# Optimization experiments

Measured on AMD Instinct MI355X. Metric: run time of the kernel, lower is better.

Reference implementation:

```python
import jax, jax.numpy as jnp
import numpy as np

BSZ, T, H, P, N = 2, 2048, 16, 64, 64

def setup_inputs() -> dict:
    key = jax.random.key(0)
    k1, k2, k3, k4, k5 = jax.random.split(key, 5)
    X = jax.random.normal(k1, (BSZ, T, H, P), dtype=jnp.float32)
    delta = jax.random.uniform(k2, (BSZ, T, H), dtype=jnp.float32)
    Bmat = jax.random.normal(k3, (BSZ, T, N), dtype=jnp.float32)
    Cmat = jax.random.normal(k4, (BSZ, T, N), dtype=jnp.float32)
    # module init: A_log = log(arange(1, n_heads+1))
    A_log = jnp.log(jnp.arange(1, H + 1, dtype=jnp.float32))
    return {"X": X, "delta": delta, "Bmat": Bmat, "Cmat": Cmat, "A_log": A_log}

def reference(X, delta, Bmat, Cmat, A_log):
    # X: [B,T,H,P], delta: [B,T,H], Bmat/Cmat: [B,T,N], A_log: [H]
    Bsz, Tlen, Hh, Pp = X.shape
    Nn = Bmat.shape[-1]
    dA = jnp.exp(delta * -jnp.exp(A_log))  # [B,T,H] per-step scalar decay

    def step(h, inp):
        dA_t, dt_t, X_t, B_t, C_t = inp  # [B,H], [B,H], [B,H,P], [B,N], [B,N]
        # outer-product input: delta * X outer B -> [B,H,P,N]
        dBx = (dt_t[:, :, None, None] * X_t[..., None]) * B_t[:, None, None, :]
        h = dA_t[:, :, None, None] * h + dBx
        y_t = jnp.einsum('bhpn,bn->bhp', h, C_t)
        return h, y_t

    h0 = jnp.zeros((Bsz, Hh, Pp, Nn), dtype=X.dtype)
    xs = (
        jnp.moveaxis(dA, 1, 0),    # [T,B,H]
        jnp.moveaxis(delta, 1, 0), # [T,B,H]
        jnp.moveaxis(X, 1, 0),     # [T,B,H,P]
        jnp.moveaxis(Bmat, 1, 0),  # [T,B,N]
        jnp.moveaxis(Cmat, 1, 0),  # [T,B,N]
    )
    h_last, ys = jax.lax.scan(step, h0, xs)
    y = jnp.moveaxis(ys, 0, 1)  # [B,T,H,P]
    return y, h_last
```

## Files before the change

### kernel.cpp

```cpp
#include <hip/hip_runtime.h>


constexpr int BSZ = 2, T = 2048, H = 16, P = 64, N = 64;
constexpr int L = 64, NC = T / L;
constexpr int LSB = 72;

using bf16x8 = __attribute__((ext_vector_type(8))) short;
using f32x4  = __attribute__((ext_vector_type(4))) float;

__device__ inline ushort f2bf(float f) {
    unsigned u = __float_as_uint(f);
    u += 0x7FFFu + ((u >> 16) & 1u);
    return (ushort)(u >> 16);
}
__device__ inline unsigned pack2(float a, float b) {
    return (unsigned)f2bf(a) | ((unsigned)f2bf(b) << 16);
}
__device__ inline float bf2f(ushort h) {
    return __uint_as_float(((unsigned)h) << 16);
}
__device__ inline int swz(int row, int col) {
    return row * 64 + ((((col >> 3) ^ (row & 7))) << 3) + (col & 7);
}

typedef __attribute__((address_space(3))) unsigned int       lds_u32;
typedef const __attribute__((address_space(1))) unsigned int glb_u32;
__device__ inline void dma16(const void* g, void* l) {
    __builtin_amdgcn_global_load_lds((glb_u32*)g, (lds_u32*)l, 16, 0, 0);
}
__device__ inline void dma4(const void* g, void* l) {
    __builtin_amdgcn_global_load_lds((glb_u32*)g, (lds_u32*)l, 4, 0, 0);
}

__global__ __launch_bounds__(256, 4) void ka_prep(
    const float* __restrict__ X, const float* __restrict__ delta,
    const float* __restrict__ Bm, const float* __restrict__ Cm,
    const float* __restrict__ A_log,
    ushort* __restrict__ Xtg, ushort* __restrict__ Hbuf,
    ushort* __restrict__ Bbf, ushort* __restrict__ Cbf,
    float* __restrict__ Vec, float* __restrict__ Dchunk)
{
    __shared__ __align__(16) ushort sXt[4096];
    __shared__ __align__(16) ushort sBt[64 * LSB];
    __shared__ float sWf[64];

    const int tid  = threadIdx.x, lane = tid & 63, w = tid >> 6;
    const int quad = lane >> 4,   l16  = lane & 15;
    const int blk = blockIdx.x;
    const int h   = blk & (H - 1);
    const int c   = (blk >> 4) & (NC - 1);
    const int b   = blk >> 9;
    const int t0  = c * L;
    const int chunkid = (b * H + h) * NC + c;
    const int bcid    = b * NC + c;

    {
        const float* gB = Bm + ((size_t)b * T + t0) * N;
        #pragma unroll
        for (int i = 0; i < 8; ++i) {
            int tau = (w * 8 + i) * 2;
            *(unsigned*)&sBt[lane * LSB + tau] =
                pack2(gB[(size_t)tau * N + lane], gB[(size_t)(tau + 1) * N + lane]);
        }
    }
    {
        const float* gX = X + (((size_t)b * T + t0) * H + h) * P;
        #pragma unroll
        for (int i = 0; i < 8; ++i) {
            int tau = w * 16 + 2 * i;
            *(unsigned*)&sXt[swz(lane, tau)] =
                pack2(gX[(size_t)tau * (H * P) + lane],
                      gX[(size_t)(tau + 1) * (H * P) + lane]);
        }
    }
    if (h == 0) {
        const float4* gB4 = (const float4*)(Bm + ((size_t)b * T + t0) * N);
        const float4* gC4 = (const float4*)(Cm + ((size_t)b * T + t0) * N);
        ushort* Bt = Bbf + (size_t)bcid * 4096;
        ushort* Ct = Cbf + (size_t)bcid * 4096;
        #pragma unroll
        for (int r = 0; r < 4; ++r) {
            int idx = r * 256 + tid, t = idx >> 4, n4 = idx & 15;
            int g = n4 >> 1, half = n4 & 1;
            int off = t * 64 + (((g ^ (t & 7))) << 3) + half * 4;
            float4 vb = gB4[idx], vc = gC4[idx];
            *(uint2*)&Bt[off] = make_uint2(pack2(vb.x, vb.y), pack2(vb.z, vb.w));
            *(uint2*)&Ct[off] = make_uint2(pack2(vc.x, vc.y), pack2(vc.z, vc.w));
        }
    }
    if (w == 0) {
        float dl = delta[((size_t)b * T + t0 + lane) * H + h];
        float s = -__expf(A_log[h]) * dl;
        #pragma unroll
        for (int off = 1; off < 64; off <<= 1) {
            float u = __shfl_up(s, off, 64);
            if (lane >= off) s += u;
        }
        float sL  = __shfl(s, 63, 64);
        float lnd = __logf(dl);
        sWf[lane] = __expf(sL + lnd - s);
        float* vp = Vec + (size_t)chunkid * 192;
        vp[lane]       = s;
        vp[64 + lane]  = lnd - s;
        vp[128 + lane] = __expf(s);
        if (lane == 63) Dchunk[chunkid] = __expf(sL);
    }
    __syncthreads();

    f32x4 ha[4];
    #pragma unroll
    for (int j = 0; j < 4; ++j) ha[j] = (f32x4){0.f, 0.f, 0.f, 0.f};
    #pragma unroll
    for (int ks = 0; ks < 2; ++ks) {
        const int ko = ks * 32 + quad * 8;
        const int sg = (ko >> 3) ^ (l16 & 7);
        bf16x8 xa = *(const bf16x8*)&sXt[(w * 16 + l16) * 64 + sg * 8];
        union { bf16x8 v; unsigned u[4]; } xw;
        #pragma unroll
        for (int j2 = 0; j2 < 4; ++j2)
            xw.u[j2] = pack2(bf2f((ushort)xa[2*j2])   * sWf[ko + 2*j2],
                             bf2f((ushort)xa[2*j2+1]) * sWf[ko + 2*j2+1]);
        #pragma unroll
        for (int jn = 0; jn < 4; ++jn) {
            bf16x8 bb = *(const bf16x8*)&sBt[(jn * 16 + l16) * LSB + ko];
            ha[jn] = __builtin_amdgcn_mfma_f32_16x16x32_bf16(xw.v, bb, ha[jn], 0, 0, 0);
        }
    }

    {
        ushort* Xtt = Xtg + (size_t)chunkid * 4096;
        #pragma unroll
        for (int i = 0; i < 2; ++i) {
            int j = i * 256 + tid;
            ((uint4*)Xtt)[j] = ((const uint4*)sXt)[j];
        }
    }
    __syncthreads();
    {
        ushort* hst = sBt;
        #pragma unroll
        for (int jn = 0; jn < 4; ++jn)
            #pragma unroll
            for (int r = 0; r < 4; ++r)
                hst[swz(w * 16 + quad * 4 + r, jn * 16 + l16)] = f2bf(ha[jn][r]);
    }
    __syncthreads();
    {
        ushort* Ht = Hbuf + (size_t)chunkid * 4096;
        #pragma unroll
        for (int i = 0; i < 2; ++i) {
            int j = i * 256 + tid;
            ((uint4*)Ht)[j] = ((const uint4*)sBt)[j];
        }
    }
}

__global__ __launch_bounds__(256, 4) void k2_scan(
    const float* __restrict__ Dchunk, ushort* __restrict__ Hbuf,
    float* __restrict__ Hlast)
{
    const unsigned gid = blockIdx.x * 256u + threadIdx.x;
    const int bh  = gid >> 11;
    const int rem = gid & 2047;
    unsigned* Hb = (unsigned*)Hbuf;
    unsigned v[NC];
    #pragma unroll
    for (int cc = 0; cc < NC; ++cc)
        v[cc] = Hb[(size_t)(bh * NC + cc) * 2048 + rem];
    float hx = 0.f, hy = 0.f;
    #pragma unroll
    for (int cc = 0; cc < NC; ++cc) {
        const float lo = bf2f((ushort)(v[cc] & 0xffffu));
        const float hi = bf2f((ushort)(v[cc] >> 16));
        v[cc] = pack2(hx, hy);
        const float D = Dchunk[bh * NC + cc];
        hx = D * hx + lo;
        hy = D * hy + hi;
    }
    #pragma unroll
    for (int cc = 0; cc < NC; ++cc)
        Hb[(size_t)(bh * NC + cc) * 2048 + rem] = v[cc];
    const int p   = rem >> 5, w32 = rem & 31;
    const int g   = (w32 >> 2) ^ (p & 7);
    const int n0  = (g << 3) + ((w32 & 3) << 1);
    *(float2*)&Hlast[(size_t)bh * 4096 + p * 64 + n0] = make_float2(hx, hy);
}

__global__ __launch_bounds__(256, 4) void k3_y(
    const ushort* __restrict__ Xtg, const ushort* __restrict__ Bbf,
    const ushort* __restrict__ Cbf, const float* __restrict__ Vec,
    const ushort* __restrict__ Hbuf, float* __restrict__ Y)
{
    __shared__ __align__(16) ushort sC [4096];
    __shared__ __align__(16) ushort sB [4096];
    __shared__ __align__(16) ushort sXt[4096];
    __shared__ __align__(16) ushort sH [4096];
    __shared__ float sVec[192];

    const int tid  = threadIdx.x, lane = tid & 63, w = tid >> 6;
    const int quad = lane >> 4,   l16  = lane & 15;
    const int blk = blockIdx.x;
    const int h   = blk & (H - 1);
    const int c   = (blk >> 4) & (NC - 1);
    const int b   = blk >> 9;
    const int t0  = c * L;
    const int chunkid = (b * H + h) * NC + c;
    const int bcid    = b * NC + c;

    {
        const ushort* gsrc;
        ushort* ldst;
        if      (w == 0) { gsrc = Cbf + (size_t)bcid * 4096;    ldst = sC;  }
        else if (w == 1) { gsrc = Bbf + (size_t)bcid * 4096;    ldst = sB;  }
        else if (w == 2) { gsrc = Xtg + (size_t)chunkid * 4096; ldst = sXt; }
        else             { gsrc = Hbuf + (size_t)chunkid * 4096; ldst = sH; }
        const char* g = (const char*)gsrc + lane * 16;
        #pragma unroll
        for (int i = 0; i < 8; ++i)
            dma16(g + i * 1024, (char*)ldst + i * 1024);
        if (w == 0) {
            const float* vp = Vec + (size_t)chunkid * 192;
            dma4(vp + lane,       sVec);
            dma4(vp + 64 + lane,  sVec + 64);
            dma4(vp + 128 + lane, sVec + 128);
        }
    }
    __syncthreads();

    f32x4 g4[4];
    #pragma unroll
    for (int j = 0; j < 4; ++j) g4[j] = (f32x4){0.f, 0.f, 0.f, 0.f};
    #pragma unroll
    for (int ks = 0; ks < 2; ++ks) {
        const int ko = ks * 32 + quad * 8;
        const int sg = (ko >> 3) ^ (l16 & 7);
        bf16x8 af = *(const bf16x8*)&sC[(w * 16 + l16) * 64 + sg * 8];
        #pragma unroll
        for (int jt = 0; jt < 4; ++jt) {
            bf16x8 bfr = *(const bf16x8*)&sB[(jt * 16 + l16) * 64 + sg * 8];
            g4[jt] = __builtin_amdgcn_mfma_f32_16x16x32_bf16(af, bfr, g4[jt], 0, 0, 0);
        }
    }
    __syncthreads();

    #pragma unroll
    for (int jt = 0; jt < 4; ++jt) {
        const int tau = jt * 16 + l16;
        const float sbv = sVec[64 + tau];
        #pragma unroll
        for (int r = 0; r < 4; ++r) {
            const int t = w * 16 + quad * 4 + r;
            float arg = (tau <= t) ? (sVec[t] + sbv) : -80.0f;
            sB[swz(t, tau)] = f2bf(__expf(arg) * g4[jt][r]);
        }
    }
    __syncthreads();

    f32x4 ya[4], acc[4];
    #pragma unroll
    for (int j = 0; j < 4; ++j) {
        ya[j]  = (f32x4){0.f, 0.f, 0.f, 0.f};
        acc[j] = (f32x4){0.f, 0.f, 0.f, 0.f};
    }
    #pragma unroll
    for (int ks = 0; ks < 2; ++ks) {
        const int ko = ks * 32 + quad * 8;
        const int sg = (ko >> 3) ^ (l16 & 7);
        bf16x8 sa = *(const bf16x8*)&sB[(w * 16 + l16) * 64 + sg * 8];
        bf16x8 ca = *(const bf16x8*)&sC[(w * 16 + l16) * 64 + sg * 8];
        #pragma unroll
        for (int jp = 0; jp < 4; ++jp) {
            bf16x8 xb = *(const bf16x8*)&sXt[(jp * 16 + l16) * 64 + sg * 8];
            bf16x8 hb = *(const bf16x8*)&sH [(jp * 16 + l16) * 64 + sg * 8];
            ya[jp]  = __builtin_amdgcn_mfma_f32_16x16x32_bf16(sa, xb, ya[jp], 0, 0, 0);
            acc[jp] = __builtin_amdgcn_mfma_f32_16x16x32_bf16(ca, hb, acc[jp], 0, 0, 0);
        }
    }

    float* Yg = Y + (((size_t)b * T + t0) * H + h) * P;
    #pragma unroll
    for (int jp = 0; jp < 4; ++jp)
        #pragma unroll
        for (int r = 0; r < 4; ++r) {
            const int t = w * 16 + quad * 4 + r;
            Yg[(size_t)t * (H * P) + jp * 16 + l16] =
                ya[jp][r] + sVec[128 + t] * acc[jp][r];
        }
}

extern "C" void kernel_launch(void* const* d_in, const int* in_sizes, int n_in,
                              void* d_out, int out_size, void* d_ws, size_t ws_size,
                              hipStream_t stream) {
    const float* X     = (const float*)d_in[0];
    const float* delta = (const float*)d_in[1];
    const float* Bm    = (const float*)d_in[2];
    const float* Cm    = (const float*)d_in[3];
    const float* A_log = (const float*)d_in[4];

    float* Y     = (float*)d_out;
    float* Hlast = (float*)d_out + (size_t)BSZ * T * H * P;

    char* ws = (char*)d_ws;
    ushort* Hbuf = (ushort*)(ws);
    ushort* Xtg  = (ushort*)(ws + (8u << 20));
    ushort* Bbf  = (ushort*)(ws + (16u << 20));
    ushort* Cbf  = (ushort*)(ws + (16u << 20) + (512u << 10));
    float*  Vec  = (float*)(ws + (17u << 20));
    float*  Dchunk = (float*)(ws + (18u << 20));

    const int nblk = BSZ * NC * H;
    ka_prep<<<nblk, 256, 0, stream>>>(X, delta, Bm, Cm, A_log,
                                      Xtg, Hbuf, Bbf, Cbf, Vec, Dchunk);
    k2_scan<<<256, 256, 0, stream>>>(Dchunk, Hbuf, Hlast);
    k3_y<<<nblk, 256, 0, stream>>>(Xtg, Bbf, Cbf, Vec, Hbuf, Y);
}
```

Measured before the change: 95.55 us.

## Fold inter-chunk state scan into the output kernel, removing separate scan launch

The separate chunk-state scan kernel is removed. Each output block now recomputes its own incoming state by accumulating the decayed per-chunk states of all earlier chunks directly from the workspace. The last chunk also produces the final hidden state. This saves a kernel launch and the global read-modify-write of the state buffer, but adds redundant work that grows with chunk index (quadratic in the number of chunks), which creates load imbalance across blocks.

```diff
diff --git a/kernel.cpp b/kernel.cpp
--- a/kernel.cpp
+++ b/kernel.cpp
@@ -137,59 +137,25 @@
     }
     __syncthreads();
     {
-        ushort* hst = sBt;
         #pragma unroll
         for (int jn = 0; jn < 4; ++jn)
             #pragma unroll
             for (int r = 0; r < 4; ++r)
-                hst[swz(w * 16 + quad * 4 + r, jn * 16 + l16)] = f2bf(ha[jn][r]);
+                sBt[swz(w * 16 + quad * 4 + r, jn * 16 + l16)] = f2bf(ha[jn][r]);
     }
     __syncthreads();
     {
         ushort* Ht = Hbuf + (size_t)chunkid * 4096;
-        #pragma unroll
-        for (int i = 0; i < 2; ++i) {
-            int j = i * 256 + tid;
-            ((uint4*)Ht)[j] = ((const uint4*)sBt)[j];
-        }
-    }
-}
-
-__global__ __launch_bounds__(256, 4) void k2_scan(
-    const float* __restrict__ Dchunk, ushort* __restrict__ Hbuf,
-    float* __restrict__ Hlast)
-{
-    const unsigned gid = blockIdx.x * 256u + threadIdx.x;
-    const int bh  = gid >> 11;
-    const int rem = gid & 2047;
-    unsigned* Hb = (unsigned*)Hbuf;
-    unsigned v[NC];
-    #pragma unroll
-    for (int cc = 0; cc < NC; ++cc)
-        v[cc] = Hb[(size_t)(bh * NC + cc) * 2048 + rem];
-    float hx = 0.f, hy = 0.f;
-    #pragma unroll
-    for (int cc = 0; cc < NC; ++cc) {
-        const float lo = bf2f((ushort)(v[cc] & 0xffffu));
-        const float hi = bf2f((ushort)(v[cc] >> 16));
-        v[cc] = pack2(hx, hy);
-        const float D = Dchunk[bh * NC + cc];
-        hx = D * hx + lo;
-        hy = D * hy + hi;
-    }
-    #pragma unroll
-    for (int cc = 0; cc < NC; ++cc)
-        Hb[(size_t)(bh * NC + cc) * 2048 + rem] = v[cc];
-    const int p   = rem >> 5, w32 = rem & 31;
-    const int g   = (w32 >> 2) ^ (p & 7);
-    const int n0  = (g << 3) + ((w32 & 3) << 1);
-    *(float2*)&Hlast[(size_t)bh * 4096 + p * 64 + n0] = make_float2(hx, hy);
+        ((uint4*)Ht)[tid]       = ((const uint4*)sBt)[tid];
+        ((uint4*)Ht)[256 + tid] = ((const uint4*)sBt)[256 + tid];
+    }
 }
 
 __global__ __launch_bounds__(256, 4) void k3_y(
     const ushort* __restrict__ Xtg, const ushort* __restrict__ Bbf,
     const ushort* __restrict__ Cbf, const float* __restrict__ Vec,
-    const ushort* __restrict__ Hbuf, float* __restrict__ Y)
+    const ushort* __restrict__ Hbuf, const float* __restrict__ Dchunk,
+    float* __restrict__ Hlast, float* __restrict__ Y)
 {
     __shared__ __align__(16) ushort sC [4096];
     __shared__ __align__(16) ushort sB [4096];
@@ -204,25 +170,78 @@
     const int c   = (blk >> 4) & (NC - 1);
     const int b   = blk >> 9;
     const int t0  = c * L;
-    const int chunkid = (b * H + h) * NC + c;
+    const int bh  = b * H + h;
+    const int chunkid = bh * NC + c;
     const int bcid    = b * NC + c;
 
     {
-        const ushort* gsrc;
-        ushort* ldst;
+        const ushort* gsrc = nullptr;
+        ushort* ldst = nullptr;
         if      (w == 0) { gsrc = Cbf + (size_t)bcid * 4096;    ldst = sC;  }
         else if (w == 1) { gsrc = Bbf + (size_t)bcid * 4096;    ldst = sB;  }
         else if (w == 2) { gsrc = Xtg + (size_t)chunkid * 4096; ldst = sXt; }
-        else             { gsrc = Hbuf + (size_t)chunkid * 4096; ldst = sH; }
-        const char* g = (const char*)gsrc + lane * 16;
-        #pragma unroll
-        for (int i = 0; i < 8; ++i)
-            dma16(g + i * 1024, (char*)ldst + i * 1024);
-        if (w == 0) {
+        if (w < 3) {
+            const char* g = (const char*)gsrc + lane * 16;
+            #pragma unroll
+            for (int i = 0; i < 8; ++i)
+                dma16(g + i * 1024, (char*)ldst + i * 1024);
+        } else {
             const float* vp = Vec + (size_t)chunkid * 192;
             dma4(vp + lane,       sVec);
             dma4(vp + 64 + lane,  sVec + 64);
             dma4(vp + 128 + lane, sVec + 128);
+        }
+    }
+
+    float hs[16];
+    #pragma unroll
+    for (int e = 0; e < 16; ++e) hs[e] = 0.f;
+    {
+        const uint4* Hb = (const uint4*)(Hbuf + (size_t)bh * NC * 4096);
+        const float* Dp = Dchunk + bh * NC;
+        #pragma unroll 4
+        for (int cc = 0; cc < c; ++cc) {
+            uint4 t0v = Hb[cc * 512 + tid];
+            uint4 t1v = Hb[cc * 512 + 256 + tid];
+            const float D = Dp[cc];
+            unsigned tin[8] = {t0v.x, t0v.y, t0v.z, t0v.w,
+                               t1v.x, t1v.y, t1v.z, t1v.w};
+            #pragma unroll
+            for (int j = 0; j < 8; ++j) {
+                hs[2*j]   = D * hs[2*j]   + bf2f((ushort)(tin[j] & 0xffffu));
+                hs[2*j+1] = D * hs[2*j+1] + bf2f((ushort)(tin[j] >> 16));
+            }
+        }
+    }
+    {
+        uint4 p0 = make_uint4(pack2(hs[0], hs[1]),  pack2(hs[2], hs[3]),
+                              pack2(hs[4], hs[5]),  pack2(hs[6], hs[7]));
+        uint4 p1 = make_uint4(pack2(hs[8], hs[9]),  pack2(hs[10], hs[11]),
+                              pack2(hs[12], hs[13]), pack2(hs[14], hs[15]));
+        ((uint4*)sH)[tid]       = p0;
+        ((uint4*)sH)[256 + tid] = p1;
+    }
+    if (c == NC - 1) {
+        const uint4* Hb = (const uint4*)(Hbuf + (size_t)bh * NC * 4096);
+        uint4 t0v = Hb[c * 512 + tid];
+        uint4 t1v = Hb[c * 512 + 256 + tid];
+        const float D = Dchunk[bh * NC + c];
+        unsigned tin[8] = {t0v.x, t0v.y, t0v.z, t0v.w,
+                           t1v.x, t1v.y, t1v.z, t1v.w};
+        float hl[16];
+        #pragma unroll
+        for (int j = 0; j < 8; ++j) {
+            hl[2*j]   = D * hs[2*j]   + bf2f((ushort)(tin[j] & 0xffffu));
+            hl[2*j+1] = D * hs[2*j+1] + bf2f((ushort)(tin[j] >> 16));
+        }
+        #pragma unroll
+        for (int q = 0; q < 2; ++q) {
+            const int u4  = q * 256 + tid;
+            const int row = u4 >> 3;
+            const int rg  = (u4 & 7) ^ (row & 7);
+            float* dst = Hlast + (size_t)bh * 4096 + row * 64 + rg * 8;
+            *(float4*)dst       = make_float4(hl[8*q+0], hl[8*q+1], hl[8*q+2], hl[8*q+3]);
+            *(float4*)(dst + 4) = make_float4(hl[8*q+4], hl[8*q+5], hl[8*q+6], hl[8*q+7]);
         }
     }
     __syncthreads();
@@ -311,6 +330,6 @@
     const int nblk = BSZ * NC * H;
     ka_prep<<<nblk, 256, 0, stream>>>(X, delta, Bm, Cm, A_log,
                                       Xtg, Hbuf, Bbf, Cbf, Vec, Dchunk);
-    k2_scan<<<256, 256, 0, stream>>>(Dchunk, Hbuf, Hlast);
-    k3_y<<<nblk, 256, 0, stream>>>(Xtg, Bbf, Cbf, Vec, Hbuf, Y);
-}
+    k3_y<<<nblk, 256, 0, stream>>>(Xtg, Bbf, Cbf, Vec, Hbuf, Dchunk,
+                                   Hlast, Y);
+}
```

After: 97.07 us. Within noise of the previous version (+1.6%).
